# Kernel optimization log

Hardware: AMD Instinct MI355X
Metric: run time of the kernel (lower is better)

Reference implementation:

```python
import jax, jax.numpy as jnp
import numpy as np

B, N, G = 8, 512, 16          # images, proposals/img, gt boxes/img
C = 91                        # num classes (incl background)
FEAT = 256 * 7 * 7            # pooled RoI feature dim = 12544
REP = 1024                    # TwoMLPHead representation size
FG, BG = 0.5, 0.5             # fg/bg IoU thresholds
BBOX_W = (10.0, 10.0, 5.0, 5.0)
BETA = 1.0 / 9.0              # smooth-L1 beta


def setup_inputs() -> dict:
    key = jax.random.key(0)
    ks = jax.random.split(key, 12)
    # valid xyxy boxes inside an ~800x800 image
    tl = jax.random.uniform(ks[0], (B, N, 2), minval=0.0, maxval=700.0)
    wh = jax.random.uniform(ks[1], (B, N, 2), minval=8.0, maxval=128.0)
    proposals = jnp.concatenate([tl, tl + wh], axis=-1)
    gtl = jax.random.uniform(ks[2], (B, G, 2), minval=0.0, maxval=700.0)
    gwh = jax.random.uniform(ks[3], (B, G, 2), minval=8.0, maxval=128.0)
    gt_boxes = jnp.concatenate([gtl, gtl + gwh], axis=-1)
    gt_labels = jax.random.randint(ks[4], (B, G), 1, C)  # foreground labels 1..C-1
    P = N + G
    features = jax.random.normal(ks[5], (B * P, FEAT), dtype=jnp.float32)
    s = 0.01
    return {
        'proposals': proposals, 'gt_boxes': gt_boxes, 'features': features,
        'W1': jax.random.normal(ks[6], (FEAT, REP), jnp.float32) * s,
        'b1': jnp.zeros((REP,), jnp.float32),
        'W2': jax.random.normal(ks[7], (REP, REP), jnp.float32) * s,
        'b2': jnp.zeros((REP,), jnp.float32),
        'Wcls': jax.random.normal(ks[8], (REP, C), jnp.float32) * s,
        'bcls': jnp.zeros((C,), jnp.float32),
        'Wbox': jax.random.normal(ks[9], (REP, C * 4), jnp.float32) * s,
        'bbox': jnp.zeros((C * 4,), jnp.float32),
        'gt_labels': gt_labels,
    }


def _box_iou(gt, pr):
    # gt: [B,G,4], pr: [B,P,4] -> [B,G,P]
    area_g = (gt[..., 2] - gt[..., 0]) * (gt[..., 3] - gt[..., 1])
    area_p = (pr[..., 2] - pr[..., 0]) * (pr[..., 3] - pr[..., 1])
    lt = jnp.maximum(gt[:, :, None, :2], pr[:, None, :, :2])
    rb = jnp.minimum(gt[:, :, None, 2:], pr[:, None, :, 2:])
    wh = jnp.clip(rb - lt, 0.0)
    inter = wh[..., 0] * wh[..., 1]
    return inter / (area_g[:, :, None] + area_p[:, None, :] - inter)


def _encode(ref, gt):
    # torchvision BoxCoder.encode_single; ref/gt: [...,4]
    wx, wy, ww, wh = BBOX_W
    ew = ref[..., 2] - ref[..., 0]; eh = ref[..., 3] - ref[..., 1]
    ex = ref[..., 0] + 0.5 * ew;    ey = ref[..., 1] + 0.5 * eh
    gw = gt[..., 2] - gt[..., 0];   gh = gt[..., 3] - gt[..., 1]
    gx = gt[..., 0] + 0.5 * gw;     gy = gt[..., 1] + 0.5 * gh
    return jnp.stack([
        wx * (gx - ex) / ew, wy * (gy - ey) / eh,
        ww * jnp.log(gw / ew), wh * jnp.log(gh / eh)], axis=-1)


def reference(proposals, gt_boxes, features, W1, b1, W2, b2, Wcls, bcls, Wbox, bbox, gt_labels):
    # add_gt_proposals
    props = jnp.concatenate([proposals, gt_boxes], axis=1)  # [B,P,4]
    # assign_targets_to_proposals (Matcher, allow_low_quality_matches=False)
    iou = _box_iou(gt_boxes, props)                          # [B,G,P]
    matched_vals = iou.max(axis=1)                           # [B,P]
    matched_idx = iou.argmax(axis=1)                         # [B,P]
    labels = jnp.take_along_axis(gt_labels, matched_idx, axis=1)
    labels = jnp.where(matched_vals < BG, 0, labels)                         # background
    labels = jnp.where((matched_vals >= BG) & (matched_vals < FG), -1, labels)  # ignore
    matched_gt = jnp.take_along_axis(gt_boxes, matched_idx[..., None], axis=1)  # [B,P,4]
    reg_targets = _encode(props, matched_gt).reshape(-1, 4)  # [R,4]
    labels = labels.reshape(-1)                               # [R]

    # TwoMLPHead + FastRCNNPredictor
    x = jax.nn.relu(features @ W1 + b1)
    x = jax.nn.relu(x @ W2 + b2)
    class_logits = x @ Wcls + bcls                            # [R,C]
    box_regression = (x @ Wbox + bbox).reshape(-1, C, 4)      # [R,C,4]

    # fastrcnn_loss (all proposals; ignored labels (-1) masked from CE)
    R = class_logits.shape[0]
    valid = (labels >= 0).astype(class_logits.dtype)
    safe_lab = jnp.clip(labels, 0, C - 1)
    logp = jax.nn.log_softmax(class_logits, axis=-1)
    nll = -jnp.take_along_axis(logp, safe_lab[:, None], axis=1)[:, 0]
    classification_loss = (nll * valid).sum() / jnp.maximum(valid.sum(), 1.0)

    pos = (labels > 0).astype(class_logits.dtype)
    pred = jnp.take_along_axis(box_regression, safe_lab[:, None, None], axis=1)[:, 0]  # [R,4]
    d = jnp.abs(pred - reg_targets)
    sl1 = jnp.where(d < BETA, 0.5 * d * d / BETA, d - 0.5 * BETA).sum(-1)
    box_loss = (sl1 * pos).sum() / R

    return jnp.stack([classification_loss, box_loss])
```

## Files before the change

### kernel.cpp

```cpp
#include <hip/hip_runtime.h>
#include <cstdint>
#include <cstddef>

#define BQ   8
#define NP   512
#define GQ   16
#define PP   528
#define RT   4224
#define CC   91
#define FEATD 12544
#define REPD 1024
#define NH   512
#define NHU  455
#define BETA (1.0f/9.0f)
#define WSC  64.0f

typedef float f32x4 __attribute__((ext_vector_type(4)));
typedef int   v8i  __attribute__((ext_vector_type(8)));
typedef float v16f __attribute__((ext_vector_type(16)));

__device__ __forceinline__ unsigned short f2bf(float f) {
  unsigned int x = __float_as_uint(f);
  unsigned int r = (x + 0x7fffu + ((x >> 16) & 1u)) >> 16;
  return (unsigned short)r;
}
__device__ __forceinline__ float bf2f(unsigned short u) {
  return __uint_as_float((unsigned int)u << 16);
}
__device__ __forceinline__ unsigned char f2fp8(float f) {
  return (unsigned char)(__builtin_amdgcn_cvt_pk_fp8_f32(f, 0.0f, 0, false) & 0xff);
}

__device__ __forceinline__ void ld_lds16(const void* g, void* l) {
  __builtin_amdgcn_global_load_lds(
      (const __attribute__((address_space(1))) void*)g,
      (__attribute__((address_space(3))) void*)l, 16, 0, 0);
}

constexpr size_t O_W1T = 0;
constexpr size_t SZ_W1T = (size_t)FEATD * REPD;
constexpr size_t O_W2T = O_W1T + SZ_W1T;
constexpr size_t SZ_W2T = (size_t)REPD * REPD;
constexpr size_t O_WH  = O_W2T + SZ_W2T;
constexpr size_t SZ_WH = (size_t)NH * REPD;
constexpr size_t O_BH  = O_WH + SZ_WH;
constexpr size_t SZ_BH = (size_t)NH * 4;
constexpr size_t O_X1  = O_BH + SZ_BH;
constexpr size_t SZ_X1 = (size_t)RT * REPD;
constexpr size_t O_X2  = O_X1 + SZ_X1;
constexpr size_t O_LAB = O_X2 + SZ_X1;
constexpr size_t O_TGT = O_LAB + (size_t)RT * 4;
constexpr size_t O_NLL = O_TGT + (size_t)RT * 16;
constexpr size_t O_VC  = O_NLL + (size_t)RT * 4;
constexpr size_t O_SL1 = O_VC + (size_t)RT * 4;
constexpr size_t O_PART = ((O_SL1 + (size_t)RT * 4) + 255) & ~(size_t)255;
constexpr size_t SZ_PART = (size_t)4 * RT * REPD * 2;
constexpr size_t O_F8 = O_PART + SZ_PART;

__device__ __forceinline__ void t32(const float* __restrict__ in, unsigned char* __restrict__ out,
                                    int K, int N, int row_off, int out_ld,
                                    int bx, int by, int t, float (*tile)[33]) {
  int tx = t & 31, ty = t >> 5;
  int n0 = bx * 32, k0 = by * 32;
#pragma unroll
  for (int i = 0; i < 4; ++i) {
    int k = k0 + ty + i * 8, n = n0 + tx;
    if (k < K && n < N) tile[ty + i * 8][tx] = in[(size_t)k * N + n];
  }
  __syncthreads();
#pragma unroll
  for (int i = 0; i < 4; ++i) {
    int n = n0 + ty + i * 8, k = k0 + tx;
    if (n < N && k < K) out[(size_t)(n + row_off) * out_ld + k] = f2fp8(tile[tx][ty + i * 8] * WSC);
  }
}

#define NB_CV ((RT * FEATD / 4) / 256)
#define NB_W1 ((REPD/32)*(FEATD/32))
#define NB_W2 ((REPD/32)*(REPD/32))
#define NB_WC (3*(REPD/32))
#define NB_WB (12*(REPD/32))
#define NB_HI 230
#define NB_MT 17
#define NB_PREP (NB_CV+NB_W1+NB_W2+NB_WC+NB_WB+NB_HI+NB_MT)

__global__ void prep(const float* __restrict__ feat, unsigned int* __restrict__ feat8,
                     const float* __restrict__ W1, const float* __restrict__ W2,
                     const float* __restrict__ Wcls, const float* __restrict__ Wbox,
                     const float* __restrict__ bcls, const float* __restrict__ bbox,
                     const float* __restrict__ proposals, const float* __restrict__ gt_boxes,
                     const int* __restrict__ gt_labels,
                     unsigned char* __restrict__ W1t, unsigned char* __restrict__ W2t,
                     unsigned char* __restrict__ Wh, float* __restrict__ bh,
                     int* __restrict__ labels, float* __restrict__ tgts) {
  __shared__ float tile[32][33];
  int b = blockIdx.x, t = threadIdx.x;
  if (b < NB_CV) {
    long i = (long)b * 256 + t;
    float4 f = ((const float4*)feat)[i];
    unsigned int r = (unsigned int)__builtin_amdgcn_cvt_pk_fp8_f32(f.x, f.y, 0, false);
    r = (unsigned int)__builtin_amdgcn_cvt_pk_fp8_f32(f.z, f.w, (int)r, true);
    feat8[i] = r;
    return;
  }
  b -= NB_CV;
  if (b < NB_W1) { t32(W1, W1t, FEATD, REPD, 0, FEATD, b % (REPD/32), b / (REPD/32), t, tile); return; }
  b -= NB_W1;
  if (b < NB_W2) { t32(W2, W2t, REPD, REPD, 0, REPD, b % 32, b / 32, t, tile); return; }
  b -= NB_W2;
  if (b < NB_WC) { t32(Wcls, Wh, REPD, CC, 0, REPD, b % 3, b / 3, t, tile); return; }
  b -= NB_WC;
  if (b < NB_WB) { t32(Wbox, Wh, REPD, 4 * CC, CC, REPD, b % 12, b / 12, t, tile); return; }
  b -= NB_WB;
  if (b < NB_HI) {
    int idx = b * 256 + t;
    const int npad = (NH - NHU) * REPD;
    if (idx < npad) Wh[(size_t)NHU * REPD + idx] = 0;
    else {
      int i2 = idx - npad;
      if (i2 < NH) bh[i2] = (i2 < CC) ? bcls[i2] : (i2 < NHU ? bbox[i2 - CC] : 0.0f);
    }
    return;
  }
  b -= NB_HI;
  int r = b * 256 + t;
  if (r >= RT) return;
  int bi_ = r / PP, p = r % PP;
  float x0, y0, x1, y1;
  if (p < NP) {
    const float* qq = proposals + ((size_t)bi_ * NP + p) * 4;
    x0 = qq[0]; y0 = qq[1]; x1 = qq[2]; y1 = qq[3];
  } else {
    const float* qq = gt_boxes + ((size_t)bi_ * GQ + (p - NP)) * 4;
    x0 = qq[0]; y0 = qq[1]; x1 = qq[2]; y1 = qq[3];
  }
  float ap = (x1 - x0) * (y1 - y0);
  float best = -1.0f; int bg = 0;
#pragma unroll
  for (int g = 0; g < GQ; ++g) {
    const float* gb = gt_boxes + ((size_t)bi_ * GQ + g) * 4;
    float gx0 = gb[0], gy0 = gb[1], gx1 = gb[2], gy1 = gb[3];
    float ag = (gx1 - gx0) * (gy1 - gy0);
    float iw = fmaxf(fminf(gx1, x1) - fmaxf(gx0, x0), 0.0f);
    float ih = fmaxf(fminf(gy1, y1) - fmaxf(gy0, y0), 0.0f);
    float inter = iw * ih;
    float iou = inter / (ag + ap - inter);
    if (iou > best) { best = iou; bg = g; }
  }
  int lab = gt_labels[bi_ * GQ + bg];
  if (best < 0.5f) lab = 0;
  labels[r] = lab;
  const float* gb = gt_boxes + ((size_t)bi_ * GQ + bg) * 4;
  float ew = x1 - x0, eh = y1 - y0;
  float ex = x0 + 0.5f * ew, ey = y0 + 0.5f * eh;
  float gw = gb[2] - gb[0], gh = gb[3] - gb[1];
  float gx = gb[0] + 0.5f * gw, gy = gb[1] + 0.5f * gh;
  tgts[r * 4 + 0] = 10.0f * (gx - ex) / ew;
  tgts[r * 4 + 1] = 10.0f * (gy - ey) / eh;
  tgts[r * 4 + 2] = 5.0f * logf(gw / ew);
  tgts[r * 4 + 3] = 5.0f * logf(gh / eh);
}

__global__ __launch_bounds__(256, 4)
void gemm_f8(const unsigned char* __restrict__ A, const unsigned char* __restrict__ Bt,
             unsigned short* __restrict__ P, int M, int Nc, int K, int Kspl,
             int n_nblk, int n_my, int npairs) {
  __shared__ unsigned char As[128 * 64];
  __shared__ unsigned char Bs[128 * 64];

  const int g = blockIdx.x;
  const int xcd = g & 7;
  const int kix = g >> 3;
  const int n  = kix % n_nblk;
  const int pi = kix / n_nblk;
  const int p  = pi * 8 + xcd;
  if (p >= npairs) return;
  const int y  = p % n_my;
  const int kz = p / n_my;
  const int m0 = y * 128, n0 = n * 128;

  const int tid = threadIdx.x;
  const int w = tid >> 6, L = tid & 63;
  const int l31 = L & 31, h = L >> 5;
  const int wr = (w >> 1) * 64, wc = (w & 1) * 64;
  const size_t kbase = (size_t)kz * Kspl;

  const int srow = L & 15, schk = (L >> 4) * 16;
  const int sg = 2 * w;
  const unsigned char* gA0 = A  + (size_t)(m0 + sg * 16 + srow) * K + kbase + schk;
  const unsigned char* gA1 = A  + (size_t)(m0 + (sg + 1) * 16 + srow) * K + kbase + schk;
  const unsigned char* gB0 = Bt + (size_t)(n0 + sg * 16 + srow) * K + kbase + schk;
  const unsigned char* gB1 = Bt + (size_t)(n0 + (sg + 1) * 16 + srow) * K + kbase + schk;
  unsigned char* lA0 = &As[sg * 1024];
  unsigned char* lA1 = &As[(sg + 1) * 1024];
  unsigned char* lB0 = &Bs[sg * 1024];
  unsigned char* lB1 = &Bs[(sg + 1) * 1024];

  int ab[2], bb[2];
#pragma unroll
  for (int i = 0; i < 2; ++i) {
    int ra = wr + i * 32 + l31;
    ab[i] = (ra >> 4) * 1024 + (ra & 15) * 16 + h * 512;
    int rb = wc + i * 32 + l31;
    bb[i] = (rb >> 4) * 1024 + (rb & 15) * 16 + h * 512;
  }

  v16f acc[2][2] = {};
  const int nk = Kspl >> 6;
  for (int kb = 0; kb < nk; ++kb) {
    const int ko = kb * 64;
    ld_lds16(gA0 + ko, lA0);
    ld_lds16(gA1 + ko, lA1);
    ld_lds16(gB0 + ko, lB0);
    ld_lds16(gB1 + ko, lB1);
    __syncthreads();
    v8i a[2], b[2];
#pragma unroll
    for (int i = 0; i < 2; ++i) {
      int4 alo = *(const int4*)&As[ab[i]];
      int4 ahi = *(const int4*)&As[ab[i] + 256];
      a[i] = (v8i){alo.x, alo.y, alo.z, alo.w, ahi.x, ahi.y, ahi.z, ahi.w};
      int4 blo = *(const int4*)&Bs[bb[i]];
      int4 bhi = *(const int4*)&Bs[bb[i] + 256];
      b[i] = (v8i){blo.x, blo.y, blo.z, blo.w, bhi.x, bhi.y, bhi.z, bhi.w};
    }
#pragma unroll
    for (int i = 0; i < 2; ++i)
#pragma unroll
      for (int j = 0; j < 2; ++j)
        acc[i][j] = __builtin_amdgcn_mfma_scale_f32_32x32x64_f8f6f4(
            a[i], b[j], acc[i][j], 0, 0, 0, 127, 0, 127);
    __syncthreads();
  }

  unsigned short* Pz = P + (size_t)kz * M * Nc;
#pragma unroll
  for (int i = 0; i < 2; ++i) {
#pragma unroll
    for (int j = 0; j < 2; ++j) {
      int colb = n0 + wc + j * 32 + l31;
#pragma unroll
      for (int r = 0; r < 16; ++r) {
        int row = m0 + wr + i * 32 + (r & 3) + 8 * (r >> 2) + 4 * h;
        Pz[(size_t)row * Nc + colb] = f2bf(acc[i][j][r]);
      }
    }
  }
}

template <int S>
__global__ void reduce_fp8k(const unsigned short* __restrict__ P, const float* __restrict__ bias,
                            unsigned int* __restrict__ outp, long MN4, int nc4) {
  long i = (long)blockIdx.x * blockDim.x + threadIdx.x;
  long stride = (long)gridDim.x * blockDim.x;
  const ushort4* P4 = (const ushort4*)P;
  const float4* B4 = (const float4*)bias;
  for (; i < MN4; i += stride) {
    float vx = 0, vy = 0, vz = 0, vw = 0;
#pragma unroll
    for (int s = 0; s < S; ++s) {
      ushort4 u = P4[s * MN4 + i];
      vx += bf2f(u.x); vy += bf2f(u.y); vz += bf2f(u.z); vw += bf2f(u.w);
    }
    float4 b = B4[i % nc4];
    vx = fmaxf(vx * (1.0f / WSC) + b.x, 0.0f);
    vy = fmaxf(vy * (1.0f / WSC) + b.y, 0.0f);
    vz = fmaxf(vz * (1.0f / WSC) + b.z, 0.0f);
    vw = fmaxf(vw * (1.0f / WSC) + b.w, 0.0f);
    unsigned int r = (unsigned int)__builtin_amdgcn_cvt_pk_fp8_f32(vx, vy, 0, false);
    r = (unsigned int)__builtin_amdgcn_cvt_pk_fp8_f32(vz, vw, (int)r, true);
    outp[i] = r;
  }
}

__global__ void loss_row(const unsigned short* __restrict__ P, const float* __restrict__ bh,
                         const int* __restrict__ labels, const float* __restrict__ tgts,
                         float* __restrict__ nll_v, float* __restrict__ vc_v,
                         float* __restrict__ sl1_v) {
  int r = blockIdx.x;
  int l = threadIdx.x;
  const size_t SL = (size_t)RT * NH;
  const unsigned short* p0 = P + (size_t)r * NH;
#define COLV(c) ((bf2f(p0[(c)]) + bf2f(p0[SL + (c)]) + bf2f(p0[2 * SL + (c)]) + \
                  bf2f(p0[3 * SL + (c)])) * (1.0f / WSC) + bh[(c)])
  float v1 = COLV(l);
  float v2 = (l < CC - 64) ? COLV(64 + l) : -3.4e38f;
  float m = fmaxf(v1, v2);
#pragma unroll
  for (int o = 32; o; o >>= 1) m = fmaxf(m, __shfl_xor(m, o));
  float e = __expf(v1 - m) + ((l < CC - 64) ? __expf(v2 - m) : 0.0f);
#pragma unroll
  for (int o = 32; o; o >>= 1) e += __shfl_xor(e, o);
  if (l == 0) {
    float lse = m + __logf(e);
    int lab = labels[r];
    int sl = lab < 0 ? 0 : (lab > CC - 1 ? CC - 1 : lab);
    float valid = (lab >= 0) ? 1.0f : 0.0f;
    nll_v[r] = (lse - COLV(sl)) * valid;
    vc_v[r] = valid;
    float s = 0.0f;
#pragma unroll
    for (int d = 0; d < 4; ++d) {
      float pd = COLV(CC + sl * 4 + d);
      float ad = fabsf(pd - tgts[r * 4 + d]);
      s += (ad < BETA) ? 0.5f * ad * ad / BETA : ad - 0.5f * BETA;
    }
    sl1_v[r] = (lab > 0) ? s : 0.0f;
  }
#undef COLV
}

__global__ void reduce_final(const float* __restrict__ nll_v, const float* __restrict__ vc_v,
                             const float* __restrict__ sl1_v, float* __restrict__ out) {
  __shared__ float s1[256], s2[256], s3[256];
  int t = threadIdx.x;
  float a = 0, b = 0, c = 0;
  for (int i = t; i < RT; i += 256) { a += nll_v[i]; b += vc_v[i]; c += sl1_v[i]; }
  s1[t] = a; s2[t] = b; s3[t] = c;
  __syncthreads();
  for (int o = 128; o; o >>= 1) {
    if (t < o) { s1[t] += s1[t + o]; s2[t] += s2[t + o]; s3[t] += s3[t + o]; }
    __syncthreads();
  }
  if (t == 0) {
    out[0] = s1[0] / fmaxf(s2[0], 1.0f);
    out[1] = s3[0] / (float)RT;
  }
}

extern "C" void kernel_launch(void* const* d_in, const int* in_sizes, int n_in,
                              void* d_out, int out_size, void* d_ws, size_t ws_size,
                              hipStream_t stream) {
  const float* proposals = (const float*)d_in[0];
  const float* gt_boxes  = (const float*)d_in[1];
  const float* features  = (const float*)d_in[2];
  const float* W1   = (const float*)d_in[3];
  const float* b1   = (const float*)d_in[4];
  const float* W2   = (const float*)d_in[5];
  const float* b2   = (const float*)d_in[6];
  const float* Wcls = (const float*)d_in[7];
  const float* bcls = (const float*)d_in[8];
  const float* Wbox = (const float*)d_in[9];
  const float* bbox = (const float*)d_in[10];
  const int* gt_labels = (const int*)d_in[11];
  float* out = (float*)d_out;

  char* ws = (char*)d_ws;
  unsigned char* W1t = (unsigned char*)(ws + O_W1T);
  unsigned char* W2t = (unsigned char*)(ws + O_W2T);
  unsigned char* Wh  = (unsigned char*)(ws + O_WH);
  float* bh          = (float*)(ws + O_BH);
  unsigned char* x1  = (unsigned char*)(ws + O_X1);
  unsigned char* x2  = (unsigned char*)(ws + O_X2);
  int* labels        = (int*)(ws + O_LAB);
  float* tgts        = (float*)(ws + O_TGT);
  float* nll_v       = (float*)(ws + O_NLL);
  float* vc_v        = (float*)(ws + O_VC);
  float* sl1_v       = (float*)(ws + O_SL1);
  unsigned short* part = (unsigned short*)(ws + O_PART);
  unsigned char* feat8 = (unsigned char*)(ws + O_F8);

  prep<<<NB_PREP, 256, 0, stream>>>(features, (unsigned int*)feat8, W1, W2, Wcls, Wbox,
                                    bcls, bbox, proposals, gt_boxes, gt_labels,
                                    W1t, W2t, Wh, bh, labels, tgts);

  gemm_f8<<<1088, 256, 0, stream>>>(feat8, W1t, part, RT, REPD, FEATD, FEATD / 4,
                                    8, 33, 132);
  reduce_fp8k<4><<<2048, 256, 0, stream>>>(part, b1, (unsigned int*)x1,
                                           (long)RT * REPD / 4, REPD / 4);

  gemm_f8<<<576, 256, 0, stream>>>(x1, W2t, part, RT, REPD, REPD, REPD / 2,
                                   8, 33, 66);
  reduce_fp8k<2><<<2048, 256, 0, stream>>>(part, b2, (unsigned int*)x2,
                                           (long)RT * REPD / 4, REPD / 4);

  gemm_f8<<<544, 256, 0, stream>>>(x2, Wh, part, RT, NH, REPD, REPD / 4,
                                   4, 33, 132);

  loss_row<<<RT, 64, 0, stream>>>(part, bh, labels, tgts, nll_v, vc_v, sl1_v);
  reduce_final<<<1, 256, 0, stream>>>(nll_v, vc_v, sl1_v, out);
}
```

Baseline: 523.7 us.

## Double-buffer LDS tiles in fp8 GEMM to overlap global loads with MFMA

Doubles the LDS tile buffers in the fp8 GEMM and prefetches the next K-slice directly into the alternate buffer while the current slice is consumed by MFMAs. Explicit vmcnt/lgkmcnt waits and raw barriers replace the __syncthreads pairs, so global-to-LDS latency can be hidden behind compute. LDS use doubles to 32KB per block, which may reduce occupancy under the 4-blocks launch bound.

```diff
diff --git a/kernel.cpp b/kernel.cpp
--- a/kernel.cpp
+++ b/kernel.cpp
@@ -165,8 +165,8 @@
 void gemm_f8(const unsigned char* __restrict__ A, const unsigned char* __restrict__ Bt,
              unsigned short* __restrict__ P, int M, int Nc, int K, int Kspl,
              int n_nblk, int n_my, int npairs) {
-  __shared__ unsigned char As[128 * 64];
-  __shared__ unsigned char Bs[128 * 64];
+  __shared__ unsigned char As[2 * 8192];
+  __shared__ unsigned char Bs[2 * 8192];
 
   const int g = blockIdx.x;
   const int xcd = g & 7;
@@ -187,14 +187,11 @@
 
   const int srow = L & 15, schk = (L >> 4) * 16;
   const int sg = 2 * w;
+  const int sgo0 = sg * 1024, sgo1 = (sg + 1) * 1024;
   const unsigned char* gA0 = A  + (size_t)(m0 + sg * 16 + srow) * K + kbase + schk;
   const unsigned char* gA1 = A  + (size_t)(m0 + (sg + 1) * 16 + srow) * K + kbase + schk;
   const unsigned char* gB0 = Bt + (size_t)(n0 + sg * 16 + srow) * K + kbase + schk;
   const unsigned char* gB1 = Bt + (size_t)(n0 + (sg + 1) * 16 + srow) * K + kbase + schk;
-  unsigned char* lA0 = &As[sg * 1024];
-  unsigned char* lA1 = &As[(sg + 1) * 1024];
-  unsigned char* lB0 = &Bs[sg * 1024];
-  unsigned char* lB1 = &Bs[(sg + 1) * 1024];
 
   int ab[2], bb[2];
 #pragma unroll
@@ -205,23 +202,38 @@
     bb[i] = (rb >> 4) * 1024 + (rb & 15) * 16 + h * 512;
   }
 
+  ld_lds16(gA0, &As[sgo0]);
+  ld_lds16(gA1, &As[sgo1]);
+  ld_lds16(gB0, &Bs[sgo0]);
+  ld_lds16(gB1, &Bs[sgo1]);
+
   v16f acc[2][2] = {};
   const int nk = Kspl >> 6;
+  int cur = 0;
   for (int kb = 0; kb < nk; ++kb) {
-    const int ko = kb * 64;
-    ld_lds16(gA0 + ko, lA0);
-    ld_lds16(gA1 + ko, lA1);
-    ld_lds16(gB0 + ko, lB0);
-    ld_lds16(gB1 + ko, lB1);
-    __syncthreads();
+    const int cb = cur << 13;
+    const int nb = cb ^ 8192;
+    if (kb + 1 < nk) {
+      const int ko = (kb + 1) * 64;
+      ld_lds16(gA0 + ko, &As[nb + sgo0]);
+      ld_lds16(gA1 + ko, &As[nb + sgo1]);
+      ld_lds16(gB0 + ko, &Bs[nb + sgo0]);
+      ld_lds16(gB1 + ko, &Bs[nb + sgo1]);
+      asm volatile("s_waitcnt vmcnt(4)" ::: "memory");
+    } else {
+      asm volatile("s_waitcnt vmcnt(0)" ::: "memory");
+    }
+    __builtin_amdgcn_sched_barrier(0);
+    __builtin_amdgcn_s_barrier();
+
     v8i a[2], b[2];
 #pragma unroll
     for (int i = 0; i < 2; ++i) {
-      int4 alo = *(const int4*)&As[ab[i]];
-      int4 ahi = *(const int4*)&As[ab[i] + 256];
+      int4 alo = *(const int4*)&As[cb + ab[i]];
+      int4 ahi = *(const int4*)&As[cb + ab[i] + 256];
       a[i] = (v8i){alo.x, alo.y, alo.z, alo.w, ahi.x, ahi.y, ahi.z, ahi.w};
-      int4 blo = *(const int4*)&Bs[bb[i]];
-      int4 bhi = *(const int4*)&Bs[bb[i] + 256];
+      int4 blo = *(const int4*)&Bs[cb + bb[i]];
+      int4 bhi = *(const int4*)&Bs[cb + bb[i] + 256];
       b[i] = (v8i){blo.x, blo.y, blo.z, blo.w, bhi.x, bhi.y, bhi.z, bhi.w};
     }
 #pragma unroll
@@ -230,7 +242,11 @@
       for (int j = 0; j < 2; ++j)
         acc[i][j] = __builtin_amdgcn_mfma_scale_f32_32x32x64_f8f6f4(
             a[i], b[j], acc[i][j], 0, 0, 0, 127, 0, 127);
-    __syncthreads();
+
+    asm volatile("s_waitcnt lgkmcnt(0)" ::: "memory");
+    __builtin_amdgcn_sched_barrier(0);
+    __builtin_amdgcn_s_barrier();
+    cur ^= 1;
   }
 
   unsigned short* Pz = P + (size_t)kz * M * Nc;
```

After: 521.9 us. About the same (-0.3%).
